# Kernel tuning notes

Measured on AMD Instinct MI355X. Metric: run time of the kernel, lower is better.

## Reference

```python
import jax, jax.numpy as jnp
import numpy as np

N = 50000      # nodes
E = 800000     # edges (avg degree 16)
IN_DIM = 256
HID = 64
HEADS = 4
OUT_DIM = 128
NEG_SLOPE = 0.2


def setup_inputs() -> dict:
    key = jax.random.key(0)
    ks = jax.random.split(key, 9)
    h = jax.random.normal(ks[0], (N, IN_DIM), jnp.float32)
    src = jax.random.randint(ks[1], (E,), 0, N, dtype=jnp.int32)
    dst = jax.random.randint(ks[2], (E,), 0, N, dtype=jnp.int32)
    # layer1: fc IN_DIM -> HEADS*HID, attn vectors [HEADS, HID]
    W1 = jax.random.normal(ks[3], (IN_DIM, HEADS * HID), jnp.float32) * (1.0 / np.sqrt(IN_DIM))
    attn_l1 = jax.random.normal(ks[4], (HEADS, HID), jnp.float32) * (1.0 / np.sqrt(HID))
    attn_r1 = jax.random.normal(ks[5], (HEADS, HID), jnp.float32) * (1.0 / np.sqrt(HID))
    # layer2: fc HEADS*HID -> 1*OUT_DIM, attn vectors [1, OUT_DIM]
    W2 = jax.random.normal(ks[6], (HEADS * HID, OUT_DIM), jnp.float32) * (1.0 / np.sqrt(HEADS * HID))
    attn_l2 = jax.random.normal(ks[7], (1, OUT_DIM), jnp.float32) * (1.0 / np.sqrt(OUT_DIM))
    attn_r2 = jax.random.normal(ks[8], (1, OUT_DIM), jnp.float32) * (1.0 / np.sqrt(OUT_DIM))
    return {"h": h, "src": src, "dst": dst,
            "W1": W1, "attn_l1": attn_l1, "attn_r1": attn_r1,
            "W2": W2, "attn_l2": attn_l2, "attn_r2": attn_r2}


def _gat_conv(h, W, attn_l, attn_r, src, dst):
    """DGL-style GATConv: returns [N, heads, out_dim]."""
    H, D = attn_l.shape
    feat = (h @ W).reshape(-1, H, D)                       # [N, H, D]
    el = jnp.einsum('nhd,hd->nh', feat, attn_l)            # [N, H]
    er = jnp.einsum('nhd,hd->nh', feat, attn_r)            # [N, H]
    e = jax.nn.leaky_relu(el[src] + er[dst], NEG_SLOPE)    # [E, H]
    # edge softmax over incoming edges of each dst node (stable)
    emax = jax.lax.stop_gradient(
        jax.ops.segment_max(e, dst, num_segments=N))       # [N, H]
    ex = jnp.exp(e - emax[dst])                            # [E, H]
    denom = jax.ops.segment_sum(ex, dst, num_segments=N)   # [N, H]
    alpha = ex / denom[dst]                                # [E, H]
    msg = alpha[:, :, None] * feat[src]                    # [E, H, D]
    return jax.ops.segment_sum(msg, dst, num_segments=N)   # [N, H, D]


def reference(h, src, dst, W1, attn_l1, attn_r1, W2, attn_l2, attn_r2):
    h1 = _gat_conv(h, W1, attn_l1, attn_r1, src, dst)      # [N, HEADS, HID]
    h1 = jax.nn.elu(h1.reshape(N, HEADS * HID))            # view + ELU
    h2 = _gat_conv(h1, W2, attn_l2, attn_r2, src, dst)     # [N, 1, OUT_DIM]
    return h2.squeeze(1)                                   # [N, OUT_DIM]
```

## Files before the change

### kernel.cpp

```cpp
#include <hip/hip_runtime.h>
#include <hip/hip_bf16.h>
#include <math.h>

#define NN 50000
#define EE 800000

__device__ __forceinline__ float lrelu(float v){ return v > 0.f ? v : 0.2f * v; }
__device__ __forceinline__ float sel4(float4 v, int h){
  return h == 0 ? v.x : h == 1 ? v.y : h == 2 ? v.z : v.w;
}
__device__ __forceinline__ ushort f2bf(float x){
  union { __hip_bfloat16 b; ushort u; } cv; cv.b = __float2bfloat16(x); return cv.u;
}
__device__ __forceinline__ float bf2f(ushort u){
  union { uint u; float f; } cv; cv.u = (uint)u << 16; return cv.f;
}

typedef __attribute__((ext_vector_type(8))) short bf16x8;
typedef __attribute__((ext_vector_type(4))) float f32x4;

__device__ __forceinline__ void gload16(const ushort* g, ushort* l){
  const auto* gp = reinterpret_cast<const __attribute__((address_space(1))) ushort*>((size_t)g);
  auto* lp = reinterpret_cast<__attribute__((address_space(3))) ushort*>((size_t)l);
  __builtin_amdgcn_global_load_lds(gp, lp, 16, 0, 0);
}

__global__ void k_hist(const int* __restrict__ dst, int* __restrict__ cnt, int E){
  int i = blockIdx.x * blockDim.x + threadIdx.x;
  if (i < E) atomicAdd(&cnt[dst[i]], 1);
}

__global__ __launch_bounds__(1024) void k_scan_bsum(const int* __restrict__ cnt, int* __restrict__ bsum, int n){
  __shared__ int ws[16];
  int t = threadIdx.x, i = blockIdx.x*1024 + t;
  int v = (i < n) ? cnt[i] : 0;
  #pragma unroll
  for (int off = 32; off; off >>= 1) v += __shfl_down(v, off);
  if ((t & 63) == 0) ws[t >> 6] = v;
  __syncthreads();
  if (t < 64){
    int x = (t < 16) ? ws[t] : 0;
    #pragma unroll
    for (int off = 32; off; off >>= 1) x += __shfl_down(x, off);
    if (t == 0) bsum[blockIdx.x] = x;
  }
}

__global__ void k_scan_boff(const int* __restrict__ bsum, int* __restrict__ boff,
                            int nb, int* __restrict__ rowptr, int n){
  int t = threadIdx.x;
  int v = (t < nb) ? bsum[t] : 0;
  int x = v;
  #pragma unroll
  for (int off = 1; off < 64; off <<= 1){ int y = __shfl_up(x, off); if (t >= off) x += y; }
  if (t < nb) boff[t] = x - v;
  if (t == 63) rowptr[n] = x;
}

__global__ __launch_bounds__(1024) void k_scan_write(const int* __restrict__ cnt, const int* __restrict__ boff,
                                                     int* __restrict__ rowptr, int n){
  __shared__ int ws[16];
  int t = threadIdx.x, w = t >> 6, lane = t & 63, i = blockIdx.x*1024 + t;
  int v = (i < n) ? cnt[i] : 0;
  int x = v;
  #pragma unroll
  for (int off = 1; off < 64; off <<= 1){ int y = __shfl_up(x, off); if (lane >= off) x += y; }
  if (lane == 63) ws[w] = x;
  __syncthreads();
  if (t < 16){
    int y = ws[t];
    #pragma unroll
    for (int off = 1; off < 16; off <<= 1){ int z = __shfl_up(y, off); if (t >= off) y += z; }
    ws[t] = y;
  }
  __syncthreads();
  if (i < n) rowptr[i] = boff[blockIdx.x] + ((w > 0) ? ws[w-1] : 0) + x - v;
}

__global__ void k_scatter(const int* __restrict__ src, const int* __restrict__ dst,
                          int* __restrict__ cursor, int* __restrict__ csr_src, int E){
  int i = blockIdx.x * blockDim.x + threadIdx.x;
  if (i < E){ int p = atomicAdd(&cursor[dst[i]], 1); csr_src[p] = src[i]; }
}

__global__ void k_prepW(const float* __restrict__ W, ushort* __restrict__ Bth,
                        ushort* __restrict__ Btl, int K, int N){
  int k = blockIdx.x, n = threadIdx.x;
  float x = W[(size_t)k*N + n];
  ushort h = f2bf(x);
  ushort l = f2bf(x - bf2f(h));
  Bth[(size_t)n*K + k] = h;
  Btl[(size_t)n*K + k] = l;
}

__global__ void k_prepA(const float* __restrict__ A, ushort* __restrict__ Ab, int total4){
  int i = blockIdx.x*blockDim.x + threadIdx.x;
  if (i >= total4) return;
  float4 v = ((const float4*)A)[i];
  ((ushort4*)Ab)[i] = make_ushort4(f2bf(v.x), f2bf(v.y), f2bf(v.z), f2bf(v.w));
}

template<int MODE>
__global__ __launch_bounds__(512, 4) void k_mgemm(
    const ushort* __restrict__ Ab,
    const ushort* __restrict__ Bth, const ushort* __restrict__ Btl,
    void* __restrict__ Cout, const float* __restrict__ avl, const float* __restrict__ avr,
    float* __restrict__ el, float* __restrict__ er, int M, int K, int N)
{
  __shared__ __align__(16) ushort sA[2][128*32];
  __shared__ __align__(16) ushort sBh[2][128*32];
  __shared__ __align__(16) ushort sBl[2][128*32];
  __shared__ float sEL[2][128], sER[2][128];
  int tid = threadIdx.x;
  int w = tid >> 6, lane = tid & 63;
  int bm = blockIdx.y*128, bn = blockIdx.x*128;
  int wm = (w & 3)*32, wn = (w >> 2)*64;
  int fr = lane & 15, fg = lane >> 4;

  int srow = 16*w + (lane >> 2);
  int skoff = (lane & 3)*8;
  int arow = bm + srow; if (arow > M-1) arow = M-1;
  const ushort* gA  = Ab  + (size_t)arow*K + skoff;
  const ushort* gBh = Bth + (size_t)(bn + srow)*K + skoff;
  const ushort* gBl = Btl + (size_t)(bn + srow)*K + skoff;
  int lslice = 16*w*32;

  const int nk = K >> 5;
  gload16(gA,  &sA[0][lslice]);
  gload16(gBh, &sBh[0][lslice]);
  gload16(gBl, &sBl[0][lslice]);
  __syncthreads();

  f32x4 acc[2][4] = {};
  for (int kt = 0; kt < nk; ++kt){
    int buf = kt & 1;
    if (kt + 1 < nk){
      int k1 = (kt + 1) << 5;
      gload16(gA + k1,  &sA[buf^1][lslice]);
      gload16(gBh + k1, &sBh[buf^1][lslice]);
      gload16(gBl + k1, &sBl[buf^1][lslice]);
    }
    bf16x8 ah[2], bh[4], bl[4];
    #pragma unroll
    for (int ti = 0; ti < 2; ++ti)
      ah[ti] = *(const bf16x8*)&sA[buf][(wm + ti*16 + fr)*32 + fg*8];
    #pragma unroll
    for (int tj = 0; tj < 4; ++tj){
      int bi = (wn + tj*16 + fr)*32 + fg*8;
      bh[tj] = *(const bf16x8*)&sBh[buf][bi];
      bl[tj] = *(const bf16x8*)&sBl[buf][bi];
    }
    #pragma unroll
    for (int ti = 0; ti < 2; ++ti)
      #pragma unroll
      for (int tj = 0; tj < 4; ++tj){
        acc[ti][tj] = __builtin_amdgcn_mfma_f32_16x16x32_bf16(ah[ti], bh[tj], acc[ti][tj], 0,0,0);
        acc[ti][tj] = __builtin_amdgcn_mfma_f32_16x16x32_bf16(ah[ti], bl[tj], acc[ti][tj], 0,0,0);
      }
    __syncthreads();
  }

  int colhead = bn + wn;
  float wl[4], wr[4];
  #pragma unroll
  for (int tj = 0; tj < 4; ++tj){
    int c = colhead + tj*16 + fr;
    wl[tj] = avl[c]; wr[tj] = avr[c];
  }
  #pragma unroll
  for (int ti = 0; ti < 2; ++ti)
    #pragma unroll
    for (int i = 0; i < 4; ++i){
      int row = bm + wm + ti*16 + fg*4 + i;
      float pl = 0.f, pr = 0.f;
      #pragma unroll
      for (int tj = 0; tj < 4; ++tj){
        float v = acc[ti][tj][i];
        pl = fmaf(v, wl[tj], pl);
        pr = fmaf(v, wr[tj], pr);
        if (row < M){
          int col = colhead + tj*16 + fr;
          if (MODE == 1) ((ushort*)Cout)[(size_t)row*256 + col] = f2bf(v);
          else           ((float*)Cout)[(size_t)row*128 + col] = v;
        }
      }
      #pragma unroll
      for (int mk = 1; mk < 16; mk <<= 1){
        pl += __shfl_xor(pl, mk);
        pr += __shfl_xor(pr, mk);
      }
      if (fr == 0){
        if (MODE == 1){
          if (row < M){ el[row*4 + (colhead >> 6)] = pl; er[row*4 + (colhead >> 6)] = pr; }
        } else {
          int lr = wm + ti*16 + fg*4 + i;
          sEL[w >> 2][lr] = pl; sER[w >> 2][lr] = pr;
        }
      }
    }
  if (MODE == 2){
    __syncthreads();
    if (tid < 128){
      int row = bm + tid;
      if (row < M){
        el[row] = sEL[0][tid] + sEL[1][tid];
        er[row] = sER[0][tid] + sER[1][tid];
      }
    }
  }
}

__global__ __launch_bounds__(256) void k_fused1(
    const int* __restrict__ rowptr, const int* __restrict__ csr_src,
    const float* __restrict__ el, const float* __restrict__ er,
    const ushort* __restrict__ featb, ushort* __restrict__ h1b)
{
  __shared__ __align__(16) float p_sh[4][64*4];
  __shared__ int si_sh[4][64];
  int w = threadIdx.x >> 6, lane = threadIdx.x & 63;
  int n = blockIdx.x*4 + w;
  if (n >= NN) return;
  int b = rowptr[n], deg = rowptr[n+1] - b;
  int h = lane >> 4;
  float4 er4 = *(const float4*)&er[n*4];
  float4 m4 = make_float4(-INFINITY,-INFINITY,-INFINITY,-INFINITY);
  float4 s4 = make_float4(0,0,0,0);
  float4 acc = make_float4(0,0,0,0);

  for (int c0 = 0; c0 < deg; c0 += 64){
    int C = min(64, deg - c0);
    int si = 0;
    float4 e4 = make_float4(-INFINITY,-INFINITY,-INFINITY,-INFINITY);
    if (lane < C){
      si = csr_src[b + c0 + lane];
      float4 l4 = *(const float4*)&el[si*4];
      e4.x = lrelu(l4.x + er4.x); e4.y = lrelu(l4.y + er4.y);
      e4.z = lrelu(l4.z + er4.z); e4.w = lrelu(l4.w + er4.w);
    }
    float4 mc = e4;
    #pragma unroll
    for (int off = 32; off; off >>= 1){
      mc.x = fmaxf(mc.x, __shfl_xor(mc.x, off));
      mc.y = fmaxf(mc.y, __shfl_xor(mc.y, off));
      mc.z = fmaxf(mc.z, __shfl_xor(mc.z, off));
      mc.w = fmaxf(mc.w, __shfl_xor(mc.w, off));
    }
    float4 mn; mn.x = fmaxf(m4.x, mc.x); mn.y = fmaxf(m4.y, mc.y);
    mn.z = fmaxf(m4.z, mc.z); mn.w = fmaxf(m4.w, mc.w);
    float4 sc; sc.x = __expf(m4.x - mn.x); sc.y = __expf(m4.y - mn.y);
    sc.z = __expf(m4.z - mn.z); sc.w = __expf(m4.w - mn.w);
    m4 = mn;
    float4 p4 = make_float4(0,0,0,0);
    if (lane < C){
      p4.x = __expf(e4.x - mn.x); p4.y = __expf(e4.y - mn.y);
      p4.z = __expf(e4.z - mn.z); p4.w = __expf(e4.w - mn.w);
    }
    float4 su = p4;
    #pragma unroll
    for (int off = 32; off; off >>= 1){
      su.x += __shfl_xor(su.x, off); su.y += __shfl_xor(su.y, off);
      su.z += __shfl_xor(su.z, off); su.w += __shfl_xor(su.w, off);
    }
    s4.x = s4.x*sc.x + su.x; s4.y = s4.y*sc.y + su.y;
    s4.z = s4.z*sc.z + su.z; s4.w = s4.w*sc.w + su.w;
    float asc = sel4(sc, h);
    acc.x *= asc; acc.y *= asc; acc.z *= asc; acc.w *= asc;
    *(float4*)&p_sh[w][lane*4] = p4;
    si_sh[w][lane] = si;
    #pragma unroll 4
    for (int j = 0; j < C; ++j){
      float a = p_sh[w][j*4 + h];
      int sj = si_sh[w][j];
      ushort4 u = *(const ushort4*)&featb[(size_t)sj*256 + lane*4];
      acc.x = fmaf(a, bf2f(u.x), acc.x); acc.y = fmaf(a, bf2f(u.y), acc.y);
      acc.z = fmaf(a, bf2f(u.z), acc.z); acc.w = fmaf(a, bf2f(u.w), acc.w);
    }
  }
  float4 o = make_float4(0,0,0,0);
  if (deg > 0){
    float rs = 1.0f / sel4(s4, h);
    o.x = acc.x * rs; o.y = acc.y * rs; o.z = acc.z * rs; o.w = acc.w * rs;
    o.x = o.x > 0.f ? o.x : expm1f(o.x);
    o.y = o.y > 0.f ? o.y : expm1f(o.y);
    o.z = o.z > 0.f ? o.z : expm1f(o.z);
    o.w = o.w > 0.f ? o.w : expm1f(o.w);
  }
  ushort4 ob = make_ushort4(f2bf(o.x), f2bf(o.y), f2bf(o.z), f2bf(o.w));
  *(ushort4*)&h1b[(size_t)n*256 + lane*4] = ob;
}

__global__ __launch_bounds__(256) void k_fused2(
    const int* __restrict__ rowptr, const int* __restrict__ csr_src,
    const float* __restrict__ el, const float* __restrict__ er,
    const float* __restrict__ feat, float* __restrict__ out)
{
  __shared__ float p_sh[4][64];
  __shared__ int si_sh[4][64];
  int w = threadIdx.x >> 6, lane = threadIdx.x & 63;
  int n = blockIdx.x*4 + w;
  if (n >= NN) return;
  int b = rowptr[n], deg = rowptr[n+1] - b;
  float er_n = er[n];
  float m = -INFINITY, s = 0.f;
  float4 acc = make_float4(0,0,0,0);
  int half = lane >> 5, l32 = lane & 31;

  for (int c0 = 0; c0 < deg; c0 += 64){
    int C = min(64, deg - c0);
    int si = 0;
    float e = -INFINITY;
    if (lane < C){
      si = csr_src[b + c0 + lane];
      e = lrelu(el[si] + er_n);
    }
    float mc = e;
    #pragma unroll
    for (int off = 32; off; off >>= 1) mc = fmaxf(mc, __shfl_xor(mc, off));
    float mn = fmaxf(m, mc);
    float scl = __expf(m - mn);
    m = mn;
    float p = (lane < C) ? __expf(e - mn) : 0.f;
    float su = p;
    #pragma unroll
    for (int off = 32; off; off >>= 1) su += __shfl_xor(su, off);
    s = s*scl + su;
    acc.x *= scl; acc.y *= scl; acc.z *= scl; acc.w *= scl;
    p_sh[w][lane] = p;
    si_sh[w][lane] = si;
    int iters = (C + 1) >> 1;
    #pragma unroll 4
    for (int it = 0; it < iters; ++it){
      int e0 = 2*it + half;
      float a = p_sh[w][e0];
      int sj = si_sh[w][e0];
      float4 f = *(const float4*)&feat[(size_t)sj*128 + l32*4];
      acc.x = fmaf(a, f.x, acc.x); acc.y = fmaf(a, f.y, acc.y);
      acc.z = fmaf(a, f.z, acc.z); acc.w = fmaf(a, f.w, acc.w);
    }
  }
  acc.x += __shfl_xor(acc.x, 32); acc.y += __shfl_xor(acc.y, 32);
  acc.z += __shfl_xor(acc.z, 32); acc.w += __shfl_xor(acc.w, 32);
  if (lane < 32){
    float4 o = make_float4(0,0,0,0);
    if (deg > 0){
      float rs = 1.0f / s;
      o.x = acc.x*rs; o.y = acc.y*rs; o.z = acc.z*rs; o.w = acc.w*rs;
    }
    *(float4*)&out[(size_t)n*128 + l32*4] = o;
  }
}

static inline size_t align256(size_t x){ return (x + 255) & ~(size_t)255; }

extern "C" void kernel_launch(void* const* d_in, const int* in_sizes, int n_in,
                              void* d_out, int out_size, void* d_ws, size_t ws_size,
                              hipStream_t stream){
  const float* h_in = (const float*)d_in[0];
  const int*   src  = (const int*)d_in[1];
  const int*   dst  = (const int*)d_in[2];
  const float* W1   = (const float*)d_in[3];
  const float* al1  = (const float*)d_in[4];
  const float* ar1  = (const float*)d_in[5];
  const float* W2   = (const float*)d_in[6];
  const float* al2  = (const float*)d_in[7];
  const float* ar2  = (const float*)d_in[8];
  float* out = (float*)d_out;

  char* ws = (char*)d_ws;
  size_t off = 0;
  ushort* Ab     = (ushort*)(ws + off); off = align256(off + (size_t)NN*256*2);
  ushort* featb  = (ushort*)(ws + off); off = align256(off + (size_t)NN*256*2);
  float* feat2   = (float*)(ws + off);  off = align256(off + (size_t)NN*128*4);
  float* el1     = (float*)(ws + off);  off = align256(off + (size_t)NN*4*4);
  float* er1     = (float*)(ws + off);  off = align256(off + (size_t)NN*4*4);
  int* rowptr    = (int*)(ws + off);    off = align256(off + (size_t)(NN+1)*4);
  int* cnt       = (int*)(ws + off);    off = align256(off + (size_t)NN*4);
  int* cursor    = (int*)(ws + off);    off = align256(off + (size_t)NN*4);
  int* csr_src   = (int*)(ws + off);    off = align256(off + (size_t)EE*4);
  ushort* Bth1   = (ushort*)(ws + off); off = align256(off + (size_t)256*256*2);
  ushort* Btl1   = (ushort*)(ws + off); off = align256(off + (size_t)256*256*2);
  ushort* Bth2   = (ushort*)(ws + off); off = align256(off + (size_t)128*256*2);
  ushort* Btl2   = (ushort*)(ws + off); off = align256(off + (size_t)128*256*2);
  int* bsum      = (int*)(ws + off);    off = align256(off + (size_t)64*4);
  int* boff      = (int*)(ws + off);    off = align256(off + (size_t)64*4);
  if (off > ws_size) return;

  ushort* h1b = Ab;
  float* el2 = el1;
  float* er2 = er1;

  const int EB = (EE + 255)/256;
  const int FB = (NN + 3)/4;
  const int NB = (NN + 1023)/1024;
  const int MT = (NN + 127)/128;

  hipMemsetAsync(cnt, 0, (size_t)NN*4, stream);
  k_hist<<<EB, 256, 0, stream>>>(dst, cnt, EE);
  k_scan_bsum<<<NB, 1024, 0, stream>>>(cnt, bsum, NN);
  k_scan_boff<<<1, 64, 0, stream>>>(bsum, boff, NB, rowptr, NN);
  k_scan_write<<<NB, 1024, 0, stream>>>(cnt, boff, rowptr, NN);
  hipMemcpyAsync(cursor, rowptr, (size_t)NN*4, hipMemcpyDeviceToDevice, stream);
  k_scatter<<<EB, 256, 0, stream>>>(src, dst, cursor, csr_src, EE);

  k_prepW<<<256, 256, 0, stream>>>(W1, Bth1, Btl1, 256, 256);
  k_prepW<<<256, 128, 0, stream>>>(W2, Bth2, Btl2, 256, 128);
  k_prepA<<<(NN*64 + 255)/256, 256, 0, stream>>>(h_in, Ab, NN*64);

  k_mgemm<1><<<dim3(2, MT), 512, 0, stream>>>(Ab, Bth1, Btl1, featb, al1, ar1, el1, er1, NN, 256, 256);
  k_fused1<<<FB, 256, 0, stream>>>(rowptr, csr_src, el1, er1, featb, h1b);

  k_mgemm<2><<<dim3(1, MT), 512, 0, stream>>>(h1b, Bth2, Btl2, feat2, al2, ar2, el2, er2, NN, 256, 128);
  k_fused2<<<FB, 256, 0, stream>>>(rowptr, csr_src, el2, er2, feat2, out);
}
```

Before: 286.2 us.

## Store layer-2 features as fp16, fuse prep kernels, drop cursor memcpy

```diff
diff --git a/kernel.cpp b/kernel.cpp
--- a/kernel.cpp
+++ b/kernel.cpp
@@ -1,5 +1,6 @@
 #include <hip/hip_runtime.h>
 #include <hip/hip_bf16.h>
+#include <hip/hip_fp16.h>
 #include <math.h>
 
 #define NN 50000
@@ -14,6 +15,12 @@
 }
 __device__ __forceinline__ float bf2f(ushort u){
   union { uint u; float f; } cv; cv.u = (uint)u << 16; return cv.f;
+}
+__device__ __forceinline__ ushort f2h(float x){
+  union { __half h; ushort u; } cv; cv.h = __float2half(x); return cv.u;
+}
+__device__ __forceinline__ float h2f(ushort u){
+  union { ushort u; __half h; } cv; cv.u = u; return __half2float(cv.h);
 }
 
 typedef __attribute__((ext_vector_type(8))) short bf16x8;
@@ -58,7 +65,7 @@
 }
 
 __global__ __launch_bounds__(1024) void k_scan_write(const int* __restrict__ cnt, const int* __restrict__ boff,
-                                                     int* __restrict__ rowptr, int n){
+                                                     int* __restrict__ rowptr, int* __restrict__ cursor, int n){
   __shared__ int ws[16];
   int t = threadIdx.x, w = t >> 6, lane = t & 63, i = blockIdx.x*1024 + t;
   int v = (i < n) ? cnt[i] : 0;
@@ -74,7 +81,11 @@
     ws[t] = y;
   }
   __syncthreads();
-  if (i < n) rowptr[i] = boff[blockIdx.x] + ((w > 0) ? ws[w-1] : 0) + x - v;
+  if (i < n){
+    int ex = boff[blockIdx.x] + ((w > 0) ? ws[w-1] : 0) + x - v;
+    rowptr[i] = ex;
+    cursor[i] = ex;
+  }
 }
 
 __global__ void k_scatter(const int* __restrict__ src, const int* __restrict__ dst,
@@ -83,21 +94,29 @@
   if (i < E){ int p = atomicAdd(&cursor[dst[i]], 1); csr_src[p] = src[i]; }
 }
 
-__global__ void k_prepW(const float* __restrict__ W, ushort* __restrict__ Bth,
-                        ushort* __restrict__ Btl, int K, int N){
-  int k = blockIdx.x, n = threadIdx.x;
-  float x = W[(size_t)k*N + n];
-  ushort h = f2bf(x);
-  ushort l = f2bf(x - bf2f(h));
-  Bth[(size_t)n*K + k] = h;
-  Btl[(size_t)n*K + k] = l;
-}
-
-__global__ void k_prepA(const float* __restrict__ A, ushort* __restrict__ Ab, int total4){
-  int i = blockIdx.x*blockDim.x + threadIdx.x;
-  if (i >= total4) return;
-  float4 v = ((const float4*)A)[i];
-  ((ushort4*)Ab)[i] = make_ushort4(f2bf(v.x), f2bf(v.y), f2bf(v.z), f2bf(v.w));
+__global__ void k_prep(const float* __restrict__ A, ushort* __restrict__ Ab,
+                       const float* __restrict__ W1, ushort* __restrict__ Bth1, ushort* __restrict__ Btl1,
+                       const float* __restrict__ W2, ushort* __restrict__ Bth2, ushort* __restrict__ Btl2){
+  int b = blockIdx.x, t = threadIdx.x;
+  if (b < 12500){
+    int i = b*256 + t;
+    float4 v = ((const float4*)A)[i];
+    ((ushort4*)Ab)[i] = make_ushort4(f2bf(v.x), f2bf(v.y), f2bf(v.z), f2bf(v.w));
+  } else if (b < 12756){
+    int k = b - 12500;
+    float x = W1[(size_t)k*256 + t];
+    ushort h = f2bf(x);
+    Bth1[(size_t)t*256 + k] = h;
+    Btl1[(size_t)t*256 + k] = f2bf(x - bf2f(h));
+  } else {
+    int k = b - 12756;
+    if (t < 128){
+      float x = W2[(size_t)k*128 + t];
+      ushort h = f2bf(x);
+      Bth2[(size_t)t*256 + k] = h;
+      Btl2[(size_t)t*256 + k] = f2bf(x - bf2f(h));
+    }
+  }
 }
 
 template<int MODE>
@@ -181,7 +200,7 @@
         if (row < M){
           int col = colhead + tj*16 + fr;
           if (MODE == 1) ((ushort*)Cout)[(size_t)row*256 + col] = f2bf(v);
-          else           ((float*)Cout)[(size_t)row*128 + col] = v;
+          else           ((ushort*)Cout)[(size_t)row*128 + col] = f2h(v);
         }
       }
       #pragma unroll
@@ -292,7 +311,7 @@
 __global__ __launch_bounds__(256) void k_fused2(
     const int* __restrict__ rowptr, const int* __restrict__ csr_src,
     const float* __restrict__ el, const float* __restrict__ er,
-    const float* __restrict__ feat, float* __restrict__ out)
+    const ushort* __restrict__ featH, float* __restrict__ out)
 {
   __shared__ float p_sh[4][64];
   __shared__ int si_sh[4][64];
@@ -333,9 +352,9 @@
       int e0 = 2*it + half;
       float a = p_sh[w][e0];
       int sj = si_sh[w][e0];
-      float4 f = *(const float4*)&feat[(size_t)sj*128 + l32*4];
-      acc.x = fmaf(a, f.x, acc.x); acc.y = fmaf(a, f.y, acc.y);
-      acc.z = fmaf(a, f.z, acc.z); acc.w = fmaf(a, f.w, acc.w);
+      ushort4 u = *(const ushort4*)&featH[(size_t)sj*128 + l32*4];
+      acc.x = fmaf(a, h2f(u.x), acc.x); acc.y = fmaf(a, h2f(u.y), acc.y);
+      acc.z = fmaf(a, h2f(u.z), acc.z); acc.w = fmaf(a, h2f(u.w), acc.w);
     }
   }
   acc.x += __shfl_xor(acc.x, 32); acc.y += __shfl_xor(acc.y, 32);
@@ -370,7 +389,7 @@
   size_t off = 0;
   ushort* Ab     = (ushort*)(ws + off); off = align256(off + (size_t)NN*256*2);
   ushort* featb  = (ushort*)(ws + off); off = align256(off + (size_t)NN*256*2);
-  float* feat2   = (float*)(ws + off);  off = align256(off + (size_t)NN*128*4);
+  ushort* feat2  = (ushort*)(ws + off); off = align256(off + (size_t)NN*128*2);
   float* el1     = (float*)(ws + off);  off = align256(off + (size_t)NN*4*4);
   float* er1     = (float*)(ws + off);  off = align256(off + (size_t)NN*4*4);
   int* rowptr    = (int*)(ws + off);    off = align256(off + (size_t)(NN+1)*4);
@@ -398,13 +417,10 @@
   k_hist<<<EB, 256, 0, stream>>>(dst, cnt, EE);
   k_scan_bsum<<<NB, 1024, 0, stream>>>(cnt, bsum, NN);
   k_scan_boff<<<1, 64, 0, stream>>>(bsum, boff, NB, rowptr, NN);
-  k_scan_write<<<NB, 1024, 0, stream>>>(cnt, boff, rowptr, NN);
-  hipMemcpyAsync(cursor, rowptr, (size_t)NN*4, hipMemcpyDeviceToDevice, stream);
+  k_scan_write<<<NB, 1024, 0, stream>>>(cnt, boff, rowptr, cursor, NN);
   k_scatter<<<EB, 256, 0, stream>>>(src, dst, cursor, csr_src, EE);
 
-  k_prepW<<<256, 256, 0, stream>>>(W1, Bth1, Btl1, 256, 256);
-  k_prepW<<<256, 128, 0, stream>>>(W2, Bth2, Btl2, 256, 128);
-  k_prepA<<<(NN*64 + 255)/256, 256, 0, stream>>>(h_in, Ab, NN*64);
+  k_prep<<<13012, 256, 0, stream>>>(h_in, Ab, W1, Bth1, Btl1, W2, Bth2, Btl2);
 
   k_mgemm<1><<<dim3(2, MT), 512, 0, stream>>>(Ab, Bth1, Btl1, featb, al1, ar1, el1, er1, NN, 256, 256);
   k_fused1<<<FB, 256, 0, stream>>>(rowptr, csr_src, el1, er1, featb, h1b);
```

Result: faster. 257.8 us (-9.9%).
